# Performance work log

Measured on AMD Instinct MI355X. Metric: run time of the kernel, lower is better.

## Reference

```python
import jax, jax.numpy as jnp
import numpy as np

B, C, T = 8, 512, 4096
KC, VC, H = 512, 512, 1  # key_channels, value_channels, num_heads
SCALE = KC // (H ** 0.5)  # faithful to original: key_channels // num_heads**0.5


def setup_inputs() -> dict:
    key = jax.random.key(0)
    k1, k2, k3, k4, k5 = jax.random.split(key, 5)
    x = jax.random.normal(k1, (B, C, T), dtype=jnp.float32)
    # 1x1 Conv1d weights: Conv1d(C, out, kernel_size=1) == per-timestep Linear
    Wqk = jax.random.normal(k2, (KC, C), dtype=jnp.float32) / np.sqrt(C)
    bqk = jax.random.normal(k3, (KC,), dtype=jnp.float32) * 0.01
    Wv = jax.random.normal(k4, (VC, C), dtype=jnp.float32) / np.sqrt(C)
    bv = jax.random.normal(k5, (VC,), dtype=jnp.float32) * 0.01
    return {"x": x, "Wqk": Wqk, "bqk": bqk, "Wv": Wv, "bv": bv}


def reference(x, Wqk, bqk, Wv, bv):
    # 1x1 conv projections: [B,C,T] -> [B,K,T] / [B,V,T]
    qk = jnp.einsum('kc,bct->bkt', Wqk, x) + bqk[None, :, None]
    val = jnp.einsum('vc,bct->bvt', Wv, x) + bv[None, :, None]
    # channel-wise attention: with num_heads=1 the reshape/transpose/matmul
    # chain reduces to scores[b,k,v] = sum_t qk[b,k,t] * val[b,v,t]
    scores = jnp.einsum('bkt,bvt->bkv', qk, val) / SCALE
    p = jax.nn.softmax(scores, axis=-1)          # softmax over value channels
    # inference path: dropout is identity (self.training == False)
    out = jnp.einsum('bkv,bvt->bkt', p, val)     # [B,K,T], K == input_channels
    return out.reshape(-1, C, T)
```

## Files before the change

kernel.cpp:

```cpp
#include <hip/hip_runtime.h>
#include <hip/hip_bf16.h>


#define BB 8
#define CC 512
#define TT 4096

typedef __attribute__((ext_vector_type(8))) short bf16x8;
typedef __attribute__((ext_vector_type(4))) short bf16x4;
typedef __attribute__((ext_vector_type(4))) float f32x4;

__device__ __forceinline__ void gload_lds16(const void* g, void* l) {
  __builtin_amdgcn_global_load_lds((const __attribute__((address_space(1))) void*)g,
                                   (__attribute__((address_space(3))) void*)l,
                                   16, 0, 0);
}
__device__ __forceinline__ float bf2f(short u) {
  return __uint_as_float(((unsigned)(unsigned short)u) << 16);
}
__device__ __forceinline__ unsigned short f2bf(float f) {
  return __builtin_bit_cast(unsigned short, __float2bfloat16(f));
}

__global__ __launch_bounds__(256)
void convert_stream_kernel(const float* __restrict__ x, __hip_bfloat16* __restrict__ xh,
                           float* __restrict__ sx)
{
  const int gid = blockIdx.x * 256 + threadIdx.x;
#pragma unroll
  for (int it = 0; it < 4; it++) {
    const int chunk = it * 524288 + gid;
    const size_t base = (size_t)chunk * 8;
    const float4 a = *(const float4*)&x[base];
    const float4 c = *(const float4*)&x[base + 4];
    bf16x8 h;
    h[0] = (short)f2bf(a.x); h[1] = (short)f2bf(a.y);
    h[2] = (short)f2bf(a.z); h[3] = (short)f2bf(a.w);
    h[4] = (short)f2bf(c.x); h[5] = (short)f2bf(c.y);
    h[6] = (short)f2bf(c.z); h[7] = (short)f2bf(c.w);
    *(bf16x8*)&xh[base] = h;
    float s = ((a.x + a.y) + (a.z + a.w)) + ((c.x + c.y) + (c.z + c.w));
#pragma unroll
    for (int off = 32; off; off >>= 1) s += __shfl_xor(s, off);
    if ((threadIdx.x & 63) == 0) atomicAdd(&sx[chunk >> 9], s);
  }
}

__global__ __launch_bounds__(256)
void prep_w_kernel(const float* __restrict__ Wqk, const float* __restrict__ Wv,
                   const float* __restrict__ sx,
                   __hip_bfloat16* __restrict__ Wqkh, __hip_bfloat16* __restrict__ Wvh,
                   __hip_bfloat16* __restrict__ WvT,
                   float* __restrict__ ta, float* __restrict__ tb)
{
  const int blk = blockIdx.x;
  if (blk < 1024) {
    int i = blk * 256 + threadIdx.x;
    Wqkh[i] = __float2bfloat16(Wqk[i]);
    float wv = Wv[i];
    Wvh[i] = __float2bfloat16(wv);
    WvT[(i & 511) * 512 + (i >> 9)] = __float2bfloat16(wv);
  } else {
    int wid = threadIdx.x >> 6, lane = threadIdx.x & 63;
    int gid = (blk - 1024) * 4 + wid;
    int which = gid >> 12;
    int rem = gid & 4095;
    int b = rem >> 9, j = rem & 511;
    const float* W = which ? Wv : Wqk;
    float s = 0.f;
#pragma unroll
    for (int i2 = 0; i2 < 8; i2++) {
      int c = lane + i2 * 64;
      s += W[j * 512 + c] * sx[b * 512 + c];
    }
#pragma unroll
    for (int off = 32; off; off >>= 1) s += __shfl_xor(s, off);
    if (lane == 0) (which ? tb : ta)[b * 512 + j] = s;
  }
}

template <int BM, int BN, int EPI>
__global__ __launch_bounds__(256)
void gemm_nt_kernel(const __hip_bfloat16* __restrict__ A, long strideA, int ldA,
                    const __hip_bfloat16* __restrict__ B, long strideB, int ldB,
                    void* __restrict__ C, long strideC, int ldC,
                    int Kslice, int nslices)
{
  constexpr int FM = BM / 32, FN = BN / 32;
  const int tid = threadIdx.x, lane = tid & 63, wid = tid >> 6;

  const int gx = gridDim.x, gy = gridDim.y;
  const int lin = blockIdx.x + gx * (blockIdx.y + gy * blockIdx.z);
  const int nwg = gx * gy * (int)gridDim.z;
  const int lin2 = (lin & 7) * (nwg >> 3) + (lin >> 3);
  const int tn = lin2 % gx;
  const int r1 = lin2 / gx;
  const int tm = r1 % gy;
  const int z  = r1 / gy;
  const int b  = z / nslices;
  const int ks = z - b * nslices;

  const __hip_bfloat16* Ab = A + (size_t)b * strideA + (size_t)(tm * BM) * ldA + (size_t)ks * Kslice;
  const __hip_bfloat16* Bb = B + (size_t)b * strideB + (size_t)(tn * BN) * ldB + (size_t)ks * Kslice;

  __shared__ __align__(16) __hip_bfloat16 sA[2][BM * 64];
  __shared__ __align__(16) __hip_bfloat16 sB[2][BN * 64];

  const int wr = wid >> 1, wc = wid & 1;

  f32x4 acc[FM][FN];
#pragma unroll
  for (int m = 0; m < FM; m++)
#pragma unroll
    for (int n = 0; n < FN; n++) acc[m][n] = (f32x4){0.f, 0.f, 0.f, 0.f};

  auto stage = [&](int buf, int k0) {
#pragma unroll
    for (int i = 0; i < BM / 32; i++) {
      int e = tid * 8 + i * 2048;
      int row = e >> 6, colg = (e & 63) ^ ((row & 7) << 3);
      gload_lds16(Ab + (size_t)row * ldA + k0 + colg, &sA[buf][wid * 512 + i * 2048]);
    }
#pragma unroll
    for (int i = 0; i < BN / 32; i++) {
      int e = tid * 8 + i * 2048;
      int row = e >> 6, colg = (e & 63) ^ ((row & 7) << 3);
      gload_lds16(Bb + (size_t)row * ldB + k0 + colg, &sB[buf][wid * 512 + i * 2048]);
    }
  };

  stage(0, 0);
  __syncthreads();
  const int nsteps = Kslice >> 6;
  for (int s = 0; s < nsteps; s++) {
    if (s + 1 < nsteps) stage((s + 1) & 1, (s + 1) << 6);
    const __hip_bfloat16* cA = sA[s & 1];
    const __hip_bfloat16* cB = sB[s & 1];
#pragma unroll
    for (int ks2 = 0; ks2 < 2; ks2++) {
      bf16x8 af[FM], bfv[FN];
      const int kb = ks2 * 32 + (lane >> 4) * 8;
#pragma unroll
      for (int m = 0; m < FM; m++) {
        int row = wr * (BM / 2) + m * 16 + (lane & 15);
        af[m] = *(const bf16x8*)&cA[row * 64 + (kb ^ ((row & 7) << 3))];
      }
#pragma unroll
      for (int n = 0; n < FN; n++) {
        int row = wc * (BN / 2) + n * 16 + (lane & 15);
        bfv[n] = *(const bf16x8*)&cB[row * 64 + (kb ^ ((row & 7) << 3))];
      }
#pragma unroll
      for (int m = 0; m < FM; m++)
#pragma unroll
        for (int n = 0; n < FN; n++)
          acc[m][n] = __builtin_amdgcn_mfma_f32_16x16x32_bf16(af[m], bfv[n], acc[m][n], 0, 0, 0);
    }
    __syncthreads();
  }

  const int rb = tm * BM + wr * (BM / 2) + ((lane >> 4) << 2);
  const int cb = tn * BN + wc * (BN / 2) + (lane & 15);
  __hip_bfloat16* Cb = (__hip_bfloat16*)C + (size_t)z * strideC;
#pragma unroll
  for (int m = 0; m < FM; m++)
#pragma unroll
    for (int n = 0; n < FN; n++)
#pragma unroll
      for (int r = 0; r < 4; r++) {
        int row = rb + m * 16 + r, col = cb + n * 16;
        Cb[(size_t)row * ldC + col] = __float2bfloat16(acc[m][n][r]);
      }
}

__global__ __launch_bounds__(256)
void reduce_g_kernel(const short* __restrict__ Gpart, short* __restrict__ Gb)
{
  const int idx = (blockIdx.x * 256 + threadIdx.x) * 8;
  const int b = idx >> 18, i = idx & 262143;
  const short* base = Gpart + ((size_t)(b * 4) << 18) + i;
  float s[8];
#pragma unroll
  for (int q = 0; q < 8; q++) s[q] = 0.f;
#pragma unroll
  for (int ks = 0; ks < 4; ks++) {
    bf16x8 v = *(const bf16x8*)(base + ((size_t)ks << 18));
#pragma unroll
    for (int q = 0; q < 8; q++) s[q] += bf2f(v[q]);
  }
  bf16x8 o;
#pragma unroll
  for (int q = 0; q < 8; q++) o[q] = (short)f2bf(s[q]);
  *(bf16x8*)(Gb + ((size_t)b << 18) + i) = o;
}

__global__ __launch_bounds__(256)
void middle_kernel(const __hip_bfloat16* __restrict__ Gh,
                   const __hip_bfloat16* __restrict__ Wqkh,
                   const __hip_bfloat16* __restrict__ Wvh,
                   const __hip_bfloat16* __restrict__ WvT,
                   const float* __restrict__ bqk, const float* __restrict__ bv,
                   const float* __restrict__ ta, const float* __restrict__ tb,
                   __hip_bfloat16* __restrict__ Mm, float* __restrict__ pb)
{
  __shared__ __align__(16) __hip_bfloat16 sW[32 * 512];
  __shared__ __align__(16) __hip_bfloat16 sT[32 * 512];
  __shared__ __align__(16) __hip_bfloat16 sB[512 * 64];
  __shared__ float red1[4][32], red2[4][32], red3[4][32];

  const int tid = threadIdx.x, lane = tid & 63, wid = tid >> 6;
  const int strip = blockIdx.x, b = blockIdx.y;
  const __hip_bfloat16* Ghb = Gh + (size_t)b * 262144;

  {
    const __hip_bfloat16* As = Wqkh + (size_t)(strip * 32) * 512;
#pragma unroll
    for (int i = 0; i < 8; i++) {
      int row = i * 4 + wid;
      int scol = (lane * 8) ^ ((row & 7) << 3);
      gload_lds16(As + row * 512 + scol, &sW[i * 2048 + wid * 512]);
    }
  }

  auto stageB = [&](const __hip_bfloat16* Bsrc, int k0) {
    const int r0 = wid * 8 + (lane >> 3);
    const int sc = k0 + 8 * ((lane & 7) ^ (lane >> 3));
#pragma unroll
    for (int i = 0; i < 16; i++)
      gload_lds16(Bsrc + (size_t)(i * 32 + r0) * 512 + sc, &sB[i * 2048 + wid * 512]);
  };

  f32x4 acc[2][8];

#define RUN_STAGE(BSRC, SX)                                                     \
  {                                                                             \
    _Pragma("unroll") for (int m = 0; m < 2; m++)                               \
      _Pragma("unroll") for (int n = 0; n < 8; n++)                             \
        acc[m][n] = (f32x4){0.f, 0.f, 0.f, 0.f};                                \
    for (int t = 0; t < 8; t++) {                                               \
      stageB(BSRC, t * 64);                                                     \
      __syncthreads();                                                          \
      _Pragma("unroll") for (int ks2 = 0; ks2 < 2; ks2++) {                     \
        const int kb = ks2 * 32 + (lane >> 4) * 8;                              \
        const int kq = t * 64 + kb;                                             \
        bf16x8 af[2], bfr[8];                                                   \
        _Pragma("unroll") for (int m = 0; m < 2; m++) {                         \
          int row = m * 16 + (lane & 15);                                       \
          af[m] = *(const bf16x8*)&SX[row * 512 + (kq ^ ((row & 7) << 3))];     \
        }                                                                       \
        _Pragma("unroll") for (int n = 0; n < 8; n++) {                         \
          int row = wid * 128 + n * 16 + (lane & 15);                           \
          bfr[n] = *(const bf16x8*)&sB[row * 64 + (kb ^ ((row & 7) << 3))];     \
        }                                                                       \
        _Pragma("unroll") for (int m = 0; m < 2; m++)                           \
          _Pragma("unroll") for (int n = 0; n < 8; n++)                         \
            acc[m][n] = __builtin_amdgcn_mfma_f32_16x16x32_bf16(af[m], bfr[n], acc[m][n], 0, 0, 0); \
      }                                                                         \
      __syncthreads();                                                          \
    }                                                                           \
  }

  RUN_STAGE(Ghb, sW);
#pragma unroll
  for (int m = 0; m < 2; m++)
#pragma unroll
    for (int n = 0; n < 8; n++)
#pragma unroll
      for (int r = 0; r < 4; r++) {
        int rowl = m * 16 + ((lane >> 4) << 2) + r;
        int col = wid * 128 + n * 16 + (lane & 15);
        sT[rowl * 512 + (col ^ ((rowl & 7) << 3))] = __float2bfloat16(acc[m][n][r]);
      }
  __syncthreads();

  RUN_STAGE(Wvh, sT);

  const float* tab = ta + b * 512;
  const float* tbb = tb + b * 512;
  float bq[2][4], tar[2][4], bvc[8], tbc[8];
#pragma unroll
  for (int m = 0; m < 2; m++)
#pragma unroll
    for (int r = 0; r < 4; r++) {
      int row = strip * 32 + m * 16 + ((lane >> 4) << 2) + r;
      bq[m][r] = bqk[row]; tar[m][r] = tab[row];
    }
#pragma unroll
  for (int n = 0; n < 8; n++) {
    int col = wid * 128 + n * 16 + (lane & 15);
    bvc[n] = bv[col]; tbc[n] = tbb[col];
  }
#pragma unroll
  for (int m = 0; m < 2; m++)
#pragma unroll
    for (int n = 0; n < 8; n++)
#pragma unroll
      for (int r = 0; r < 4; r++)
        acc[m][n][r] = (acc[m][n][r] + bq[m][r] * tbc[n] + tar[m][r] * bvc[n]
                        + 4096.0f * bq[m][r] * bvc[n]) * (1.0f / 512.0f);

#pragma unroll
  for (int m = 0; m < 2; m++)
#pragma unroll
    for (int r = 0; r < 4; r++) {
      float v = acc[m][0][r];
#pragma unroll
      for (int n = 1; n < 8; n++) v = fmaxf(v, acc[m][n][r]);
#pragma unroll
      for (int off = 1; off < 16; off <<= 1) v = fmaxf(v, __shfl_xor(v, off));
      if ((lane & 15) == 0) red1[wid][m * 16 + ((lane >> 4) << 2) + r] = v;
    }
  __syncthreads();

#pragma unroll
  for (int m = 0; m < 2; m++)
#pragma unroll
    for (int r = 0; r < 4; r++) {
      int lr = m * 16 + ((lane >> 4) << 2) + r;
      float mx = fmaxf(fmaxf(red1[0][lr], red1[1][lr]), fmaxf(red1[2][lr], red1[3][lr]));
      float s = 0.f, pbp = 0.f;
#pragma unroll
      for (int n = 0; n < 8; n++) {
        float e = __expf(acc[m][n][r] - mx);
        acc[m][n][r] = e;
        s += e;
        pbp += e * bvc[n];
      }
#pragma unroll
      for (int off = 1; off < 16; off <<= 1) {
        s += __shfl_xor(s, off);
        pbp += __shfl_xor(pbp, off);
      }
      if ((lane & 15) == 0) { red2[wid][lr] = s; red3[wid][lr] = pbp; }
    }
  __syncthreads();

#pragma unroll
  for (int m = 0; m < 2; m++)
#pragma unroll
    for (int r = 0; r < 4; r++) {
      int lr = m * 16 + ((lane >> 4) << 2) + r;
      float inv = 1.0f / (red2[0][lr] + red2[1][lr] + red2[2][lr] + red2[3][lr]);
      if (wid == 0 && (lane & 15) == 0)
        pb[b * 512 + strip * 32 + lr] =
            (red3[0][lr] + red3[1][lr] + red3[2][lr] + red3[3][lr]) * inv;
#pragma unroll
      for (int n = 0; n < 8; n++) {
        int col = wid * 128 + n * 16 + (lane & 15);
        sT[lr * 512 + (col ^ ((lr & 7) << 3))] = __float2bfloat16(acc[m][n][r] * inv);
      }
    }
  __syncthreads();

  RUN_STAGE(WvT, sT);
#undef RUN_STAGE

  __hip_bfloat16* Mb = Mm + (size_t)b * 262144 + (size_t)(strip * 32) * 512;
#pragma unroll
  for (int m = 0; m < 2; m++)
#pragma unroll
    for (int n = 0; n < 8; n++)
#pragma unroll
      for (int r = 0; r < 4; r++) {
        int rowl = m * 16 + ((lane >> 4) << 2) + r;
        int col = wid * 128 + n * 16 + (lane & 15);
        Mb[rowl * 512 + col] = __float2bfloat16(acc[m][n][r]);
      }
}

__global__ __launch_bounds__(256)
void gemm_out_kernel(const __hip_bfloat16* __restrict__ Mall,
                     const __hip_bfloat16* __restrict__ xh,
                     const float* __restrict__ pball,
                     float* __restrict__ out)
{
  __shared__ __align__(16) __hip_bfloat16 sA[2][128 * 64];
  __shared__ __align__(16) __hip_bfloat16 sB[2][64 * 128];

  const int tid = threadIdx.x, lane = tid & 63, wid = tid >> 6;
  const int wr = wid >> 1, wc = wid & 1;

  const int lin = blockIdx.x + 32 * (blockIdx.y + 4 * blockIdx.z);
  const int lin2 = (lin & 7) * 128 + (lin >> 3);
  const int tn = lin2 & 31;
  const int tm = (lin2 >> 5) & 3;
  const int b  = lin2 >> 7;

  const __hip_bfloat16* Ab = Mall + (size_t)b * 262144 + (size_t)(tm * 128) * 512;
  const __hip_bfloat16* Bb = xh + (size_t)b * ((size_t)CC * TT) + tn * 128;

  f32x4 acc[4][4];
#pragma unroll
  for (int m = 0; m < 4; m++)
#pragma unroll
    for (int n = 0; n < 4; n++) acc[m][n] = (f32x4){0.f, 0.f, 0.f, 0.f};

  auto stage = [&](int buf, int k0) {
#pragma unroll
    for (int i = 0; i < 4; i++) {
      int e = tid * 8 + i * 2048;
      int row = e >> 6, colg = (e & 63) ^ ((row & 7) << 3);
      gload_lds16(Ab + (size_t)row * 512 + k0 + colg, &sA[buf][wid * 512 + i * 2048]);
    }
#pragma unroll
    for (int q = 0; q < 4; q++) {
      int E = q * 2048 + tid * 8;
      int v = ((E >> 9) << 2) | ((E >> 4) & 3);
      int t = (((E >> 6) & 7) << 4) | (E & 8);
      gload_lds16(Bb + (size_t)(k0 + v) * TT + t, &sB[buf][wid * 512 + q * 2048]);
    }
  };

  const unsigned sB32 =
      (unsigned)(size_t)(__attribute__((address_space(3))) __hip_bfloat16*)&sB[0][0];
  const unsigned btr_lo = sB32 + (lane >> 4) * 2048 + (lane & 15) * 8 + wc * 512;
  const unsigned btr_hi = btr_lo + 8192;

#define COMPUTE(BUF)                                                            \
  {                                                                             \
    _Pragma("unroll")                                                           \
    for (int ks2 = 0; ks2 < 2; ks2++) {                                         \
      bf16x8 af[4]; bf16x4 blo[4], bhi[4];                                      \
      const int kb = ks2 * 32 + (lane >> 4) * 8;                                \
      _Pragma("unroll")                                                         \
      for (int m = 0; m < 4; m++) {                                             \
        int row = wr * 64 + m * 16 + (lane & 15);                               \
        af[m] = *(const bf16x8*)&sA[BUF][row * 64 + (kb ^ ((row & 7) << 3))];   \
      }                                                                         \
      unsigned ab = ks2 ? btr_hi : btr_lo;                                      \
      _Pragma("unroll")                                                         \
      for (int n = 0; n < 4; n++) {                                             \
        asm volatile("ds_read_b64_tr_b16 %0, %1 offset:%2"                      \
                     : "=v"(blo[n]) : "v"(ab), "i"((BUF) * 16384 + n * 128));   \
        asm volatile("ds_read_b64_tr_b16 %0, %1 offset:%2"                      \
                     : "=v"(bhi[n]) : "v"(ab), "i"((BUF) * 16384 + n * 128 + 1024)); \
      }                                                                         \
      asm volatile("s_waitcnt lgkmcnt(0)" ::: "memory");                        \
      __builtin_amdgcn_sched_barrier(0);                                        \
      _Pragma("unroll")                                                         \
      for (int m = 0; m < 4; m++)                                               \
        _Pragma("unroll")                                                       \
        for (int n = 0; n < 4; n++) {                                           \
          bf16x8 b8 = __builtin_shufflevector(blo[n], bhi[n], 0, 1, 2, 3, 4, 5, 6, 7); \
          acc[m][n] = __builtin_amdgcn_mfma_f32_16x16x32_bf16(af[m], b8, acc[m][n], 0, 0, 0); \
        }                                                                       \
    }                                                                           \
  }

  stage(0, 0);
  __syncthreads();
#pragma unroll 1
  for (int s = 0; s < 8; s += 2) {
    if (s + 1 < 8) stage(1, (s + 1) * 64);
    COMPUTE(0);
    __syncthreads();
    if (s + 2 < 8) stage(0, (s + 2) * 64);
    COMPUTE(1);
    __syncthreads();
  }
#undef COMPUTE

  const int rb = tm * 128 + wr * 64 + ((lane >> 4) << 2);
  const int cb = tn * 128 + wc * 64 + (lane & 15);
  float* Cf = out + (size_t)b * ((size_t)CC * TT);
  const float* pbv = pball + b * 512;
#pragma unroll
  for (int m = 0; m < 4; m++)
#pragma unroll
    for (int n = 0; n < 4; n++)
#pragma unroll
      for (int r = 0; r < 4; r++) {
        int row = rb + m * 16 + r, col = cb + n * 16;
        Cf[(size_t)row * TT + col] = acc[m][n][r] + pbv[row];
      }
}

extern "C" void kernel_launch(void* const* d_in, const int* in_sizes, int n_in,
                              void* d_out, int out_size, void* d_ws, size_t ws_size,
                              hipStream_t stream)
{
  const float* x   = (const float*)d_in[0];
  const float* Wqk = (const float*)d_in[1];
  const float* bqk = (const float*)d_in[2];
  const float* Wv  = (const float*)d_in[3];
  const float* bv  = (const float*)d_in[4];
  float* out = (float*)d_out;

  char* w = (char*)d_ws;
  auto alloc = [&](size_t bytes) {
    void* pp = (void*)w;
    w += (bytes + 255) & ~(size_t)255;
    return pp;
  };
  __hip_bfloat16* xh     = (__hip_bfloat16*)alloc((size_t)BB * CC * TT * 2);
  short*          Gpart  = (short*)alloc((size_t)BB * 4 * CC * CC * 2);
  short*          Gb     = (short*)alloc((size_t)BB * CC * CC * 2);
  __hip_bfloat16* Mm     = (__hip_bfloat16*)alloc((size_t)BB * CC * CC * 2);
  __hip_bfloat16* Wqkh   = (__hip_bfloat16*)alloc((size_t)CC * CC * 2);
  __hip_bfloat16* Wvh    = (__hip_bfloat16*)alloc((size_t)CC * CC * 2);
  __hip_bfloat16* WvT    = (__hip_bfloat16*)alloc((size_t)CC * CC * 2);
  float* sx = (float*)alloc((size_t)BB * CC * 4);
  float* ta = (float*)alloc((size_t)BB * CC * 4);
  float* tb = (float*)alloc((size_t)BB * CC * 4);
  float* pb = (float*)alloc((size_t)BB * CC * 4);

  hipMemsetAsync(sx, 0, (size_t)BB * CC * 4, stream);

  convert_stream_kernel<<<2048, 256, 0, stream>>>(x, xh, sx);
  prep_w_kernel<<<3072, 256, 0, stream>>>(Wqk, Wv, sx, Wqkh, Wvh, WvT, ta, tb);

  const long sXH = (long)CC * TT;
  const long sSq = (long)CC * CC;

  gemm_nt_kernel<128, 128, 0><<<dim3(4, 4, BB * 4), 256, 0, stream>>>(
      xh, sXH, TT, xh, sXH, TT, Gpart, sSq, CC, 1024, 4);
  reduce_g_kernel<<<(BB * CC * CC) / (256 * 8), 256, 0, stream>>>(Gpart, Gb);

  middle_kernel<<<dim3(16, BB), 256, 0, stream>>>(
      (const __hip_bfloat16*)Gb, Wqkh, Wvh, WvT, bqk, bv, ta, tb, Mm, pb);

  gemm_out_kernel<<<dim3(32, 4, 8), 256, 0, stream>>>(Mm, xh, pb, out);
}
```

Before: 215.2 us.

## Split middle kernel into 16-row strips with double-buffered B staging

Result: slower. 220.1 us (+2.3%).

```diff
diff --git a/kernel.cpp b/kernel.cpp
--- a/kernel.cpp
+++ b/kernel.cpp
@@ -203,58 +203,52 @@
                    const float* __restrict__ ta, const float* __restrict__ tb,
                    __hip_bfloat16* __restrict__ Mm, float* __restrict__ pb)
 {
-  __shared__ __align__(16) __hip_bfloat16 sW[32 * 512];
-  __shared__ __align__(16) __hip_bfloat16 sT[32 * 512];
-  __shared__ __align__(16) __hip_bfloat16 sB[512 * 64];
-  __shared__ float red1[4][32], red2[4][32], red3[4][32];
+  __shared__ __align__(16) __hip_bfloat16 sW[16 * 512];
+  __shared__ __align__(16) __hip_bfloat16 sT[16 * 512];
+  __shared__ __align__(16) __hip_bfloat16 sB[2][512 * 32];
+  __shared__ float red1[4][16], red2[4][16], red3[4][16];
 
   const int tid = threadIdx.x, lane = tid & 63, wid = tid >> 6;
-  const int strip = blockIdx.x, b = blockIdx.y;
+  const int lin = blockIdx.x;
+  const int lin2 = (lin & 7) * 32 + (lin >> 3);
+  const int strip = lin2 & 31, b = lin2 >> 5;
   const __hip_bfloat16* Ghb = Gh + (size_t)b * 262144;
 
-  {
-    const __hip_bfloat16* As = Wqkh + (size_t)(strip * 32) * 512;
+#pragma unroll
+  for (int i = 0; i < 4; i++) {
+    int row = i * 4 + wid;
+    int scol = 8 * (lane ^ (row & 7));
+    gload_lds16(Wqkh + (size_t)(strip * 16 + row) * 512 + scol, &sW[i * 2048 + wid * 512]);
+  }
+
+  auto stageB = [&](int buf, const __hip_bfloat16* Bsrc, int k0) {
 #pragma unroll
     for (int i = 0; i < 8; i++) {
-      int row = i * 4 + wid;
-      int scol = (lane * 8) ^ ((row & 7) << 3);
-      gload_lds16(As + row * 512 + scol, &sW[i * 2048 + wid * 512]);
-    }
-  }
-
-  auto stageB = [&](const __hip_bfloat16* Bsrc, int k0) {
-    const int r0 = wid * 8 + (lane >> 3);
-    const int sc = k0 + 8 * ((lane & 7) ^ (lane >> 3));
-#pragma unroll
-    for (int i = 0; i < 16; i++)
-      gload_lds16(Bsrc + (size_t)(i * 32 + r0) * 512 + sc, &sB[i * 2048 + wid * 512]);
+      int r = i * 64 + wid * 16 + (lane >> 2);
+      int scol = k0 + 8 * ((lane & 3) ^ (r & 3));
+      gload_lds16(Bsrc + (size_t)r * 512 + scol, &sB[buf][i * 2048 + wid * 512]);
+    }
   };
 
-  f32x4 acc[2][8];
+  const int arow = lane & 15;
+  const int asw = (arow & 7) << 3;
+  f32x4 acc[8];
 
 #define RUN_STAGE(BSRC, SX)                                                     \
   {                                                                             \
-    _Pragma("unroll") for (int m = 0; m < 2; m++)                               \
-      _Pragma("unroll") for (int n = 0; n < 8; n++)                             \
-        acc[m][n] = (f32x4){0.f, 0.f, 0.f, 0.f};                                \
-    for (int t = 0; t < 8; t++) {                                               \
-      stageB(BSRC, t * 64);                                                     \
-      __syncthreads();                                                          \
-      _Pragma("unroll") for (int ks2 = 0; ks2 < 2; ks2++) {                     \
-        const int kb = ks2 * 32 + (lane >> 4) * 8;                              \
-        const int kq = t * 64 + kb;                                             \
-        bf16x8 af[2], bfr[8];                                                   \
-        _Pragma("unroll") for (int m = 0; m < 2; m++) {                         \
-          int row = m * 16 + (lane & 15);                                       \
-          af[m] = *(const bf16x8*)&SX[row * 512 + (kq ^ ((row & 7) << 3))];     \
-        }                                                                       \
-        _Pragma("unroll") for (int n = 0; n < 8; n++) {                         \
-          int row = wid * 128 + n * 16 + (lane & 15);                           \
-          bfr[n] = *(const bf16x8*)&sB[row * 64 + (kb ^ ((row & 7) << 3))];     \
-        }                                                                       \
-        _Pragma("unroll") for (int m = 0; m < 2; m++)                           \
-          _Pragma("unroll") for (int n = 0; n < 8; n++)                         \
-            acc[m][n] = __builtin_amdgcn_mfma_f32_16x16x32_bf16(af[m], bfr[n], acc[m][n], 0, 0, 0); \
+    _Pragma("unroll") for (int n = 0; n < 8; n++) acc[n] = (f32x4){0.f,0.f,0.f,0.f}; \
+    stageB(0, BSRC, 0);                                                         \
+    __syncthreads();                                                            \
+    for (int t = 0; t < 16; t++) {                                              \
+      if (t < 15) stageB((t + 1) & 1, BSRC, (t + 1) * 32);                      \
+      const __hip_bfloat16* cB = sB[t & 1];                                     \
+      const int kq = t * 32 + (lane >> 4) * 8;                                  \
+      bf16x8 af = *(const bf16x8*)&SX[arow * 512 + (kq ^ asw)];                 \
+      const int kb = (lane >> 4) * 8;                                           \
+      _Pragma("unroll") for (int n = 0; n < 8; n++) {                           \
+        int brow = wid * 128 + n * 16 + (lane & 15);                            \
+        bf16x8 bfv = *(const bf16x8*)&cB[brow * 32 + (kb ^ ((brow & 3) << 3))]; \
+        acc[n] = __builtin_amdgcn_mfma_f32_16x16x32_bf16(af, bfv, acc[n], 0, 0, 0); \
       }                                                                         \
       __syncthreads();                                                          \
     }                                                                           \
@@ -262,110 +256,103 @@
 
   RUN_STAGE(Ghb, sW);
 #pragma unroll
-  for (int m = 0; m < 2; m++)
-#pragma unroll
-    for (int n = 0; n < 8; n++)
-#pragma unroll
-      for (int r = 0; r < 4; r++) {
-        int rowl = m * 16 + ((lane >> 4) << 2) + r;
-        int col = wid * 128 + n * 16 + (lane & 15);
-        sT[rowl * 512 + (col ^ ((rowl & 7) << 3))] = __float2bfloat16(acc[m][n][r]);
-      }
+  for (int n = 0; n < 8; n++)
+#pragma unroll
+    for (int r = 0; r < 4; r++) {
+      int lr = ((lane >> 4) << 2) + r;
+      int col = wid * 128 + n * 16 + (lane & 15);
+      sT[lr * 512 + (col ^ ((lr & 7) << 3))] = __float2bfloat16(acc[n][r]);
+    }
   __syncthreads();
 
   RUN_STAGE(Wvh, sT);
 
   const float* tab = ta + b * 512;
   const float* tbb = tb + b * 512;
-  float bq[2][4], tar[2][4], bvc[8], tbc[8];
-#pragma unroll
-  for (int m = 0; m < 2; m++)
-#pragma unroll
-    for (int r = 0; r < 4; r++) {
-      int row = strip * 32 + m * 16 + ((lane >> 4) << 2) + r;
-      bq[m][r] = bqk[row]; tar[m][r] = tab[row];
-    }
+  float bvc[8], tbc[8];
 #pragma unroll
   for (int n = 0; n < 8; n++) {
     int col = wid * 128 + n * 16 + (lane & 15);
     bvc[n] = bv[col]; tbc[n] = tbb[col];
   }
-#pragma unroll
-  for (int m = 0; m < 2; m++)
-#pragma unroll
-    for (int n = 0; n < 8; n++)
-#pragma unroll
-      for (int r = 0; r < 4; r++)
-        acc[m][n][r] = (acc[m][n][r] + bq[m][r] * tbc[n] + tar[m][r] * bvc[n]
-                        + 4096.0f * bq[m][r] * bvc[n]) * (1.0f / 512.0f);
-
-#pragma unroll
-  for (int m = 0; m < 2; m++)
+  float bq[4], tar[4];
+#pragma unroll
+  for (int r = 0; r < 4; r++) {
+    int gr = strip * 16 + ((lane >> 4) << 2) + r;
+    bq[r] = bqk[gr]; tar[r] = tab[gr];
+  }
+#pragma unroll
+  for (int n = 0; n < 8; n++)
+#pragma unroll
+    for (int r = 0; r < 4; r++)
+      acc[n][r] = (acc[n][r] + bq[r] * tbc[n] + tar[r] * bvc[n]
+                   + 4096.0f * bq[r] * bvc[n]) * (1.0f / 512.0f);
+
+#pragma unroll
+  for (int r = 0; r < 4; r++) {
+    float v = acc[0][r];
+#pragma unroll
+    for (int n = 1; n < 8; n++) v = fmaxf(v, acc[n][r]);
+#pragma unroll
+    for (int off = 1; off < 16; off <<= 1) v = fmaxf(v, __shfl_xor(v, off));
+    if ((lane & 15) == 0) red1[wid][((lane >> 4) << 2) + r] = v;
+  }
+  __syncthreads();
+  float mx[4];
+#pragma unroll
+  for (int r = 0; r < 4; r++) {
+    int lr = ((lane >> 4) << 2) + r;
+    mx[r] = fmaxf(fmaxf(red1[0][lr], red1[1][lr]), fmaxf(red1[2][lr], red1[3][lr]));
+  }
+#pragma unroll
+  for (int r = 0; r < 4; r++) {
+    float s = 0.f, pp = 0.f;
+#pragma unroll
+    for (int n = 0; n < 8; n++) {
+      float e = __expf(acc[n][r] - mx[r]);
+      acc[n][r] = e;
+      s += e; pp += e * bvc[n];
+    }
+#pragma unroll
+    for (int off = 1; off < 16; off <<= 1) { s += __shfl_xor(s, off); pp += __shfl_xor(pp, off); }
+    if ((lane & 15) == 0) {
+      red2[wid][((lane >> 4) << 2) + r] = s;
+      red3[wid][((lane >> 4) << 2) + r] = pp;
+    }
+  }
+  __syncthreads();
+  float inv[4];
+#pragma unroll
+  for (int r = 0; r < 4; r++) {
+    int lr = ((lane >> 4) << 2) + r;
+    float sum = red2[0][lr] + red2[1][lr] + red2[2][lr] + red2[3][lr];
+    inv[r] = 1.0f / sum;
+    if (wid == 0 && (lane & 15) == 0)
+      pb[b * 512 + strip * 16 + lr] =
+          (red3[0][lr] + red3[1][lr] + red3[2][lr] + red3[3][lr]) * inv[r];
+  }
+#pragma unroll
+  for (int n = 0; n < 8; n++)
 #pragma unroll
     for (int r = 0; r < 4; r++) {
-      float v = acc[m][0][r];
-#pragma unroll
-      for (int n = 1; n < 8; n++) v = fmaxf(v, acc[m][n][r]);
-#pragma unroll
-      for (int off = 1; off < 16; off <<= 1) v = fmaxf(v, __shfl_xor(v, off));
-      if ((lane & 15) == 0) red1[wid][m * 16 + ((lane >> 4) << 2) + r] = v;
-    }
-  __syncthreads();
-
-#pragma unroll
-  for (int m = 0; m < 2; m++)
-#pragma unroll
-    for (int r = 0; r < 4; r++) {
-      int lr = m * 16 + ((lane >> 4) << 2) + r;
-      float mx = fmaxf(fmaxf(red1[0][lr], red1[1][lr]), fmaxf(red1[2][lr], red1[3][lr]));
-      float s = 0.f, pbp = 0.f;
-#pragma unroll
-      for (int n = 0; n < 8; n++) {
-        float e = __expf(acc[m][n][r] - mx);
-        acc[m][n][r] = e;
-        s += e;
-        pbp += e * bvc[n];
-      }
-#pragma unroll
-      for (int off = 1; off < 16; off <<= 1) {
-        s += __shfl_xor(s, off);
-        pbp += __shfl_xor(pbp, off);
-      }
-      if ((lane & 15) == 0) { red2[wid][lr] = s; red3[wid][lr] = pbp; }
-    }
-  __syncthreads();
-
-#pragma unroll
-  for (int m = 0; m < 2; m++)
-#pragma unroll
-    for (int r = 0; r < 4; r++) {
-      int lr = m * 16 + ((lane >> 4) << 2) + r;
-      float inv = 1.0f / (red2[0][lr] + red2[1][lr] + red2[2][lr] + red2[3][lr]);
-      if (wid == 0 && (lane & 15) == 0)
-        pb[b * 512 + strip * 32 + lr] =
-            (red3[0][lr] + red3[1][lr] + red3[2][lr] + red3[3][lr]) * inv;
-#pragma unroll
-      for (int n = 0; n < 8; n++) {
-        int col = wid * 128 + n * 16 + (lane & 15);
-        sT[lr * 512 + (col ^ ((lr & 7) << 3))] = __float2bfloat16(acc[m][n][r] * inv);
-      }
+      int lr = ((lane >> 4) << 2) + r;
+      int col = wid * 128 + n * 16 + (lane & 15);
+      sT[lr * 512 + (col ^ ((lr & 7) << 3))] = __float2bfloat16(acc[n][r] * inv[r]);
     }
   __syncthreads();
 
   RUN_STAGE(WvT, sT);
 #undef RUN_STAGE
 
-  __hip_bfloat16* Mb = Mm + (size_t)b * 262144 + (size_t)(strip * 32) * 512;
-#pragma unroll
-  for (int m = 0; m < 2; m++)
-#pragma unroll
-    for (int n = 0; n < 8; n++)
-#pragma unroll
-      for (int r = 0; r < 4; r++) {
-        int rowl = m * 16 + ((lane >> 4) << 2) + r;
-        int col = wid * 128 + n * 16 + (lane & 15);
-        Mb[rowl * 512 + col] = __float2bfloat16(acc[m][n][r]);
-      }
+  __hip_bfloat16* Mb = Mm + (size_t)b * 262144 + (size_t)(strip * 16) * 512;
+#pragma unroll
+  for (int n = 0; n < 8; n++)
+#pragma unroll
+    for (int r = 0; r < 4; r++) {
+      int lr = ((lane >> 4) << 2) + r;
+      int col = wid * 128 + n * 16 + (lane & 15);
+      Mb[(size_t)lr * 512 + col] = __float2bfloat16(acc[n][r]);
+    }
 }
 
 __global__ __launch_bounds__(256)
@@ -382,8 +369,8 @@
 
   const int lin = blockIdx.x + 32 * (blockIdx.y + 4 * blockIdx.z);
   const int lin2 = (lin & 7) * 128 + (lin >> 3);
-  const int tn = lin2 & 31;
-  const int tm = (lin2 >> 5) & 3;
+  const int tm = lin2 & 3;
+  const int tn = (lin2 >> 2) & 31;
   const int b  = lin2 >> 7;
 
   const __hip_bfloat16* Ab = Mall + (size_t)b * 262144 + (size_t)(tm * 128) * 512;
@@ -516,7 +503,7 @@
       xh, sXH, TT, xh, sXH, TT, Gpart, sSq, CC, 1024, 4);
   reduce_g_kernel<<<(BB * CC * CC) / (256 * 8), 256, 0, stream>>>(Gpart, Gb);
 
-  middle_kernel<<<dim3(16, BB), 256, 0, stream>>>(
+  middle_kernel<<<256, 256, 0, stream>>>(
       (const __hip_bfloat16*)Gb, Wqkh, Wvh, WvT, bqk, bv, ta, tb, Mm, pb);
 
   gemm_out_kernel<<<dim3(32, 4, 8), 256, 0, stream>>>(Mm, xh, pb, out);
```
